# Kernel tuning notes

Hardware: AMD Instinct MI355X
Metric: run time of the kernel (lower is better)

Reference implementation:

```python
import jax, jax.numpy as jnp
import numpy as np

HEADS = 12
HEAD_SIZE = 64
NEG_BIG = 1e12


def _rope_sincos(n, head_size, dtype):
    # rotary position embeddings: (n, head_size) each, with each freq repeated twice
    pos = jnp.arange(n, dtype=dtype)
    inv = jnp.power(10000.0, -2.0 * jnp.arange(head_size // 2, dtype=dtype) / head_size)
    emb = pos[:, None] * inv[None, :]               # (n, head_size//2)
    sin = jnp.repeat(jnp.sin(emb), 2, axis=-1)       # (n, head_size)
    cos = jnp.repeat(jnp.cos(emb), 2, axis=-1)
    return sin, cos


def _rotate_half(x):
    # stack([-x[...,1::2], x[...,::2]], -1).reshape_as(x)
    x2 = jnp.stack([-x[..., 1::2], x[..., ::2]], axis=-1)
    return x2.reshape(x.shape)


def setup_inputs() -> dict:
    key = jax.random.key(0)
    k1, k2, k3 = jax.random.split(key, 3)
    b, n, h = 16, 512, 1024
    inputs = jax.random.normal(k1, (b, n, h), dtype=jnp.float32)
    attention_mask = jnp.ones((b, n), dtype=jnp.float32)
    W1 = jax.random.normal(k2, (h, 2 * HEAD_SIZE), dtype=jnp.float32) * (1.0 / np.sqrt(h))
    b1 = jnp.zeros((2 * HEAD_SIZE,), dtype=jnp.float32)
    W2 = jax.random.normal(k3, (2 * HEAD_SIZE, 2 * HEADS), dtype=jnp.float32) * (1.0 / np.sqrt(2 * HEAD_SIZE))
    b2 = jnp.zeros((2 * HEADS,), dtype=jnp.float32)
    return {"inputs": inputs, "attention_mask": attention_mask,
            "W1": W1, "b1": b1, "W2": W2, "b2": b2}


def reference(inputs, attention_mask, W1, b1, W2, b2):
    b, n, _ = inputs.shape
    x = inputs @ W1 + b1                              # (b, n, 2*head_size)
    qw, kw = x[..., ::2], x[..., 1::2]                # (b, n, head_size)

    sin, cos = _rope_sincos(n, HEAD_SIZE, x.dtype)    # (n, head_size)
    qw = qw * cos[None] + _rotate_half(qw) * sin[None]
    kw = kw * cos[None] + _rotate_half(kw) * sin[None]

    logits = jnp.einsum('bmd,bnd->bmn', qw, kw) / (HEAD_SIZE ** 0.5)  # (b, n, n)

    bias = (x @ W2 + b2).transpose(0, 2, 1) / 2.0     # (b, 2*heads, n)
    logits = logits[:, None] + bias[:, ::2, None, :] + bias[:, 1::2, :, None]  # (b, heads, n, n)

    attn = 1.0 - attention_mask[:, None, None, :] * attention_mask[:, None, :, None]
    logits = logits - attn * NEG_BIG

    tril = jnp.tril(jnp.ones((n, n), dtype=logits.dtype), k=-1)
    logits = logits - tril[None, None] * NEG_BIG
    return logits
```

## Files before the change

kernel.cpp:

```cpp
#include <hip/hip_runtime.h>
#include <math.h>

#define NB 16
#define SEQ 512
#define HID 1024
#define XDIM 128
#define NHEADS 12
#define NROWS (NB*SEQ)
#define NEG_BIG 1000000000000.0f
#define MTILE 16

typedef __bf16 bf16x8 __attribute__((ext_vector_type(8)));
typedef __bf16 bf16x4 __attribute__((ext_vector_type(4)));
typedef float  f32x4  __attribute__((ext_vector_type(4)));

__global__ __launch_bounds__(256) void egp_prep(
    const float* __restrict__ W1, __bf16* __restrict__ W1T)
{
    int idx = blockIdx.x * 256 + threadIdx.x;
    int n   = idx >> 7;
    int k0  = (idx & 127) << 3;
    bf16x8 o;
    #pragma unroll
    for (int j = 0; j < 8; j++)
        o[j] = (__bf16)W1[(size_t)(k0 + j) * XDIM + n];
    *(bf16x8*)(W1T + (size_t)n * HID + k0) = o;
}

__global__ __launch_bounds__(256) void egp_stage1(
    const float* __restrict__ inp,
    const __bf16* __restrict__ W1T,
    const float* __restrict__ b1,
    const float* __restrict__ W2,
    const float* __restrict__ b2,
    __bf16* __restrict__ qw,
    __bf16* __restrict__ kw,
    float* __restrict__ biasw)
{
    __shared__ __bf16 As[2048];
    __shared__ float  Xs[MTILE][132];
    __shared__ float  W2s[XDIM * 24];
    __shared__ float  b2s[24];

    const int t    = threadIdx.x;
    const int row0 = blockIdx.x * MTILE;
    const int lane = t & 63;
    const int w    = t >> 6;
    const int quad = lane >> 4;
    const int mrow = lane & 15;
    const int ncol0 = w * 32;

    for (int i = t; i < XDIM * 24; i += 256) W2s[i] = W2[i];
    if (t < 24) b2s[t] = b2[t];

    const int m_st = t >> 4;
    const int k_st = (t & 15) * 4;
    const int s_st  = k_st >> 5;
    const int q_st  = (k_st & 31) >> 3;
    const int j_st  = k_st & 7;
    const int off_st = s_st * 1024 + q_st * 128 + m_st * 8 + j_st;
    const float* aptr = inp + (size_t)(row0 + m_st) * HID + k_st;

    float4 v[16];
    #pragma unroll
    for (int c = 0; c < 16; c++)
        v[c] = *(const float4*)(aptr + 64 * c);

    f32x4 acc0 = {0.f, 0.f, 0.f, 0.f};
    f32x4 acc1 = {0.f, 0.f, 0.f, 0.f};

    #pragma unroll
    for (int c = 0; c < 16; c++) {
        const int kc = c * 64;
        __syncthreads();
        bf16x4 p;
        p[0] = (__bf16)v[c].x; p[1] = (__bf16)v[c].y;
        p[2] = (__bf16)v[c].z; p[3] = (__bf16)v[c].w;
        *(bf16x4*)(&As[off_st]) = p;
        __syncthreads();

        #pragma unroll
        for (int s2 = 0; s2 < 2; s2++) {
            bf16x8 a = *(bf16x8*)(&As[s2 * 1024 + quad * 128 + mrow * 8]);
            {
                const __bf16* bp = W1T + (size_t)(ncol0 + mrow) * HID
                                 + kc + s2 * 32 + quad * 8;
                bf16x8 b = *(const bf16x8*)(bp);
                acc0 = __builtin_amdgcn_mfma_f32_16x16x32_bf16(a, b, acc0, 0, 0, 0);
            }
            {
                const __bf16* bp = W1T + (size_t)(ncol0 + 16 + mrow) * HID
                                 + kc + s2 * 32 + quad * 8;
                bf16x8 b = *(const bf16x8*)(bp);
                acc1 = __builtin_amdgcn_mfma_f32_16x16x32_bf16(a, b, acc1, 0, 0, 0);
            }
        }
    }

    float b1v0 = b1[ncol0 + mrow];
    float b1v1 = b1[ncol0 + 16 + mrow];
    #pragma unroll
    for (int r = 0; r < 4; r++) {
        Xs[quad * 4 + r][ncol0 + mrow]      = acc0[r] + b1v0;
        Xs[quad * 4 + r][ncol0 + 16 + mrow] = acc1[r] + b1v1;
    }
    __syncthreads();

    const int tx = t & 15;
    const int r  = t >> 4;
    const float LOG1E4 = 9.210340371976184f;
    float inv0 = expf(-((float)(2 * tx)     * (1.0f / 32.0f)) * LOG1E4);
    float inv1 = expf(-((float)(2 * tx + 1) * (1.0f / 32.0f)) * LOG1E4);
    {
        int grow  = row0 + r;
        float pos = (float)(grow & (SEQ - 1));
        float x[8];
        #pragma unroll
        for (int j = 0; j < 8; j++) x[j] = Xs[r][tx * 8 + j];
        float s0 = sinf(pos * inv0), c0 = cosf(pos * inv0);
        float s1 = sinf(pos * inv1), c1 = cosf(pos * inv1);
        bf16x4 q4, k4;
        q4[0] = (__bf16)(x[0] * c0 - x[2] * s0);
        q4[1] = (__bf16)(x[2] * c0 + x[0] * s0);
        q4[2] = (__bf16)(x[4] * c1 - x[6] * s1);
        q4[3] = (__bf16)(x[6] * c1 + x[4] * s1);
        k4[0] = (__bf16)(x[1] * c0 - x[3] * s0);
        k4[1] = (__bf16)(x[3] * c0 + x[1] * s0);
        k4[2] = (__bf16)(x[5] * c1 - x[7] * s1);
        k4[3] = (__bf16)(x[7] * c1 + x[5] * s1);
        *(bf16x4*)(qw + (size_t)grow * 64 + tx * 4) = q4;
        *(bf16x4*)(kw + (size_t)grow * 64 + tx * 4) = k4;
    }

    for (int o = t; o < MTILE * 24; o += 256) {
        int row = o / 24;
        int jj  = o - row * 24;
        float s = 0.0f;
        for (int kk = 0; kk < XDIM; kk++)
            s += Xs[row][kk] * W2s[kk * 24 + jj];
        biasw[(size_t)(row0 + row) * 24 + jj] = (s + b2s[jj]) * 0.5f;
    }
}

__global__ __launch_bounds__(256) void egp_stage2(
    const __bf16* __restrict__ qw,
    const __bf16* __restrict__ kw,
    const float* __restrict__ biasw,
    const float* __restrict__ am,
    float* __restrict__ out)
{
    __shared__ float Vals[64][68];
    __shared__ float bEs[12][64];
    __shared__ float bOs[12][64];
    __shared__ float amN[64];
    __shared__ float amM[64];

    const int b  = blockIdx.z;
    const int m0 = blockIdx.y * 64;
    const int n0 = blockIdx.x * 64;
    const int t  = threadIdx.x;
    const int lane = t & 63;
    const int w    = t >> 6;
    const int quad = lane >> 4;
    const int l16  = lane & 15;

    for (int o = t; o < 768; o += 256) {
        int nn = o & 63;
        int h  = o >> 6;
        bEs[h][nn] = biasw[(size_t)(b * SEQ + n0 + nn) * 24 + 2 * h];
        bOs[h][nn] = biasw[(size_t)(b * SEQ + m0 + nn) * 24 + 2 * h + 1];
    }
    if (t < 64)       amN[t]      = am[b * SEQ + n0 + t];
    else if (t < 128) amM[t - 64] = am[b * SEQ + m0 + (t - 64)];

    const __bf16* qbase = qw + ((size_t)(b * SEQ + m0 + w * 16 + l16)) * 64 + quad * 8;
    bf16x8 a0 = *(const bf16x8*)(qbase);
    bf16x8 a1 = *(const bf16x8*)(qbase + 32);

    f32x4 acc[4];
    #pragma unroll
    for (int nt = 0; nt < 4; nt++) {
        const __bf16* kbase = kw + ((size_t)(b * SEQ + n0 + nt * 16 + l16)) * 64 + quad * 8;
        bf16x8 b0 = *(const bf16x8*)(kbase);
        bf16x8 b1 = *(const bf16x8*)(kbase + 32);
        f32x4 z = {0.f, 0.f, 0.f, 0.f};
        z = __builtin_amdgcn_mfma_f32_16x16x32_bf16(a0, b0, z, 0, 0, 0);
        z = __builtin_amdgcn_mfma_f32_16x16x32_bf16(a1, b1, z, 0, 0, 0);
        acc[nt] = z;
    }

    #pragma unroll
    for (int nt = 0; nt < 4; nt++)
        #pragma unroll
        for (int r = 0; r < 4; r++)
            Vals[w * 16 + quad * 4 + r][nt * 16 + l16] = acc[nt][r];
    __syncthreads();

    const int tx = t & 15;
    const int ty = t >> 4;

    float amMv[4], amNv[4];
    #pragma unroll
    for (int i = 0; i < 4; i++) amMv[i] = amM[ty * 4 + i];
    #pragma unroll
    for (int j = 0; j < 4; j++) amNv[j] = amN[tx * 4 + j];

    float vals[4][4];
    #pragma unroll
    for (int i = 0; i < 4; i++) {
        int m = m0 + ty * 4 + i;
        float4 v4 = *(const float4*)(&Vals[ty * 4 + i][tx * 4]);
        float qk[4] = {v4.x, v4.y, v4.z, v4.w};
        #pragma unroll
        for (int j = 0; j < 4; j++) {
            int n = n0 + tx * 4 + j;
            float msk = (1.0f - amMv[i] * amNv[j]) * NEG_BIG
                      + ((n < m) ? NEG_BIG : 0.0f);
            vals[i][j] = qk[j] * 0.125f - msk;
        }
    }

    for (int h = 0; h < NHEADS; h++) {
        float be[4], bo[4];
        #pragma unroll
        for (int j = 0; j < 4; j++) be[j] = bEs[h][tx * 4 + j];
        #pragma unroll
        for (int i = 0; i < 4; i++) bo[i] = bOs[h][ty * 4 + i];
        float* obase = out + ((size_t)((b * NHEADS + h) * SEQ + m0 + ty * 4)) * SEQ + n0 + tx * 4;
        #pragma unroll
        for (int i = 0; i < 4; i++) {
            float4 o4;
            o4.x = vals[i][0] + be[0] + bo[i];
            o4.y = vals[i][1] + be[1] + bo[i];
            o4.z = vals[i][2] + be[2] + bo[i];
            o4.w = vals[i][3] + be[3] + bo[i];
            *(float4*)(obase + (size_t)i * SEQ) = o4;
        }
    }
}

extern "C" void kernel_launch(void* const* d_in, const int* in_sizes, int n_in,
                              void* d_out, int out_size, void* d_ws, size_t ws_size,
                              hipStream_t stream) {
    const float* inp = (const float*)d_in[0];
    const float* am  = (const float*)d_in[1];
    const float* W1  = (const float*)d_in[2];
    const float* b1  = (const float*)d_in[3];
    const float* W2  = (const float*)d_in[4];
    const float* b2  = (const float*)d_in[5];
    float* out = (float*)d_out;

    __bf16* qw   = (__bf16*)d_ws;
    __bf16* kw   = qw + (size_t)NROWS * 64;
    float*  bias = (float*)(kw + (size_t)NROWS * 64);
    __bf16* w1t  = (__bf16*)(bias + (size_t)NROWS * 24);

    egp_prep<<<64, 256, 0, stream>>>(W1, w1t);
    egp_stage1<<<NROWS / MTILE, 256, 0, stream>>>(inp, w1t, b1, W2, b2, qw, kw, bias);

    dim3 g2(SEQ / 64, SEQ / 64, NB);
    egp_stage2<<<g2, 256, 0, stream>>>(qw, kw, bias, am, out);
}
```

Baseline: 265.6 us.

## Retile stage2 to full-row 16x512 blocks with contiguous per-head row writes

Stage2 blocks now each cover 16 query rows across the full 512-key sequence instead of a 64x64 tile. Each of the four waves computes 8 MFMA tiles, and the masking is applied before the values go to shared memory. The output loop then writes each head's 16x512 slab as fully contiguous float4 rows, which should improve write coalescing on this store-bound kernel. In exchange, each block reloads the full even-bias vector (12x512) and all K rows, and uses about 60KB of LDS, which may reduce occupancy.

```diff
diff --git a/kernel.cpp b/kernel.cpp
--- a/kernel.cpp
+++ b/kernel.cpp
@@ -149,92 +149,83 @@
     const float* __restrict__ am,
     float* __restrict__ out)
 {
-    __shared__ float Vals[64][68];
-    __shared__ float bEs[12][64];
-    __shared__ float bOs[12][64];
-    __shared__ float amN[64];
-    __shared__ float amM[64];
-
-    const int b  = blockIdx.z;
-    const int m0 = blockIdx.y * 64;
-    const int n0 = blockIdx.x * 64;
+    __shared__ float Vals[MTILE][516];
+    __shared__ float bEs[NHEADS][512];
+    __shared__ float bOs[NHEADS][MTILE];
+    __shared__ float amN[512];
+    __shared__ float amM[MTILE];
+
+    const int b  = blockIdx.y;
+    const int m0 = blockIdx.x * MTILE;
     const int t  = threadIdx.x;
     const int lane = t & 63;
     const int w    = t >> 6;
     const int quad = lane >> 4;
     const int l16  = lane & 15;
 
-    for (int o = t; o < 768; o += 256) {
-        int nn = o & 63;
-        int h  = o >> 6;
-        bEs[h][nn] = biasw[(size_t)(b * SEQ + n0 + nn) * 24 + 2 * h];
-        bOs[h][nn] = biasw[(size_t)(b * SEQ + m0 + nn) * 24 + 2 * h + 1];
-    }
-    if (t < 64)       amN[t]      = am[b * SEQ + n0 + t];
-    else if (t < 128) amM[t - 64] = am[b * SEQ + m0 + (t - 64)];
-
-    const __bf16* qbase = qw + ((size_t)(b * SEQ + m0 + w * 16 + l16)) * 64 + quad * 8;
+    #pragma unroll
+    for (int u = 0; u < 2; u++) amN[t + 256 * u] = am[b * SEQ + t + 256 * u];
+    if (t < MTILE) amM[t] = am[b * SEQ + m0 + t];
+    for (int o = t; o < NHEADS * MTILE; o += 256) {
+        int h  = o >> 4;
+        int mm = o & 15;
+        bOs[h][mm] = biasw[(size_t)(b * SEQ + m0 + mm) * 24 + 2 * h + 1];
+    }
+    for (int o = t; o < NHEADS * 512; o += 256) {
+        int h = o >> 9;
+        int n = o & 511;
+        bEs[h][n] = biasw[(size_t)(b * SEQ + n) * 24 + 2 * h];
+    }
+
+    const __bf16* qbase = qw + ((size_t)(b * SEQ + m0 + l16)) * 64 + quad * 8;
     bf16x8 a0 = *(const bf16x8*)(qbase);
     bf16x8 a1 = *(const bf16x8*)(qbase + 32);
 
-    f32x4 acc[4];
-    #pragma unroll
-    for (int nt = 0; nt < 4; nt++) {
-        const __bf16* kbase = kw + ((size_t)(b * SEQ + n0 + nt * 16 + l16)) * 64 + quad * 8;
+    f32x4 acc[8];
+    #pragma unroll
+    for (int u = 0; u < 8; u++) {
+        int nt = w * 8 + u;
+        const __bf16* kbase = kw + ((size_t)(b * SEQ + nt * 16 + l16)) * 64 + quad * 8;
         bf16x8 b0 = *(const bf16x8*)(kbase);
         bf16x8 b1 = *(const bf16x8*)(kbase + 32);
         f32x4 z = {0.f, 0.f, 0.f, 0.f};
         z = __builtin_amdgcn_mfma_f32_16x16x32_bf16(a0, b0, z, 0, 0, 0);
         z = __builtin_amdgcn_mfma_f32_16x16x32_bf16(a1, b1, z, 0, 0, 0);
-        acc[nt] = z;
-    }
-
-    #pragma unroll
-    for (int nt = 0; nt < 4; nt++)
-        #pragma unroll
-        for (int r = 0; r < 4; r++)
-            Vals[w * 16 + quad * 4 + r][nt * 16 + l16] = acc[nt][r];
+        acc[u] = z;
+    }
+
+    #pragma unroll
+    for (int u = 0; u < 8; u++) {
+        int n = w * 128 + u * 16 + l16;
+        float an = amN[n];
+        #pragma unroll
+        for (int r = 0; r < 4; r++) {
+            int mloc = quad * 4 + r;
+            int m    = m0 + mloc;
+            float msk = (1.0f - amM[mloc] * an) * NEG_BIG
+                      + ((n < m) ? NEG_BIG : 0.0f);
+            Vals[mloc][n] = acc[u][r] * 0.125f - msk;
+        }
+    }
     __syncthreads();
 
-    const int tx = t & 15;
-    const int ty = t >> 4;
-
-    float amMv[4], amNv[4];
-    #pragma unroll
-    for (int i = 0; i < 4; i++) amMv[i] = amM[ty * 4 + i];
-    #pragma unroll
-    for (int j = 0; j < 4; j++) amNv[j] = amN[tx * 4 + j];
-
-    float vals[4][4];
-    #pragma unroll
-    for (int i = 0; i < 4; i++) {
-        int m = m0 + ty * 4 + i;
-        float4 v4 = *(const float4*)(&Vals[ty * 4 + i][tx * 4]);
-        float qk[4] = {v4.x, v4.y, v4.z, v4.w};
-        #pragma unroll
-        for (int j = 0; j < 4; j++) {
-            int n = n0 + tx * 4 + j;
-            float msk = (1.0f - amMv[i] * amNv[j]) * NEG_BIG
-                      + ((n < m) ? NEG_BIG : 0.0f);
-            vals[i][j] = qk[j] * 0.125f - msk;
-        }
-    }
-
+    #pragma unroll
     for (int h = 0; h < NHEADS; h++) {
-        float be[4], bo[4];
-        #pragma unroll
-        for (int j = 0; j < 4; j++) be[j] = bEs[h][tx * 4 + j];
-        #pragma unroll
-        for (int i = 0; i < 4; i++) bo[i] = bOs[h][ty * 4 + i];
-        float* obase = out + ((size_t)((b * NHEADS + h) * SEQ + m0 + ty * 4)) * SEQ + n0 + tx * 4;
-        #pragma unroll
-        for (int i = 0; i < 4; i++) {
+        float* hbase = out + ((size_t)((b * NHEADS + h) * SEQ + m0)) * SEQ;
+        #pragma unroll
+        for (int it = 0; it < 8; it++) {
+            int f4   = t + 256 * it;
+            int row  = f4 >> 7;
+            int col4 = f4 & 127;
+            float4 v = *(const float4*)(&Vals[row][col4 * 4]);
+            float4 e = *(const float4*)(&bEs[h][col4 * 4]);
+            float  bo = bOs[h][row];
             float4 o4;
-            o4.x = vals[i][0] + be[0] + bo[i];
-            o4.y = vals[i][1] + be[1] + bo[i];
-            o4.z = vals[i][2] + be[2] + bo[i];
-            o4.w = vals[i][3] + be[3] + bo[i];
-            *(float4*)(obase + (size_t)i * SEQ) = o4;
+            o4.x = v.x + e.x + bo;
+            o4.y = v.y + e.y + bo;
+            o4.z = v.z + e.z + bo;
+            o4.w = v.w + e.w + bo;
+            *(float4*)(hbase + (size_t)f4 * 4) = o4;
         }
     }
 }
@@ -258,6 +249,6 @@
     egp_prep<<<64, 256, 0, stream>>>(W1, w1t);
     egp_stage1<<<NROWS / MTILE, 256, 0, stream>>>(inp, w1t, b1, W2, b2, qw, kw, bias);
 
-    dim3 g2(SEQ / 64, SEQ / 64, NB);
+    dim3 g2(SEQ / MTILE, NB);
     egp_stage2<<<g2, 256, 0, stream>>>(qw, kw, bias, am, out);
 }
```

After: 262.6 us. No clear change (-1.1%).
